# Kernel optimization log

Hardware: AMD Instinct MI355X
Metric: run time of the kernel (lower is better)

Reference implementation:

```python
import jax, jax.numpy as jnp
import numpy as np

ALPHA = 0.2  # LeakyReLU negative slope
NEG_INF = -9e15


def setup_inputs() -> dict:
    key = jax.random.key(0)
    k1, k2, k3, k4 = jax.random.split(key, 4)
    B, T, N, Fin, Fout = 16, 12, 512, 64, 64
    h = jax.random.normal(k1, (B, T, N, Fin), dtype=jnp.float32)
    adj = jax.random.randint(k2, (N, N), 0, 2).astype(jnp.float32)
    W = jax.random.normal(k3, (Fin, Fout), dtype=jnp.float32) * 0.1
    a = jax.random.normal(k4, (2 * Fout, 1), dtype=jnp.float32) * 0.1
    return {"h": h, "adj": adj, "W": W, "a": a}


def reference(h, adj, W, a):
    # h: [B,T,N,Fin], adj: [N,N], W: [Fin,Fout], a: [2*Fout,1]
    Fout = W.shape[1]
    Wh = jnp.einsum('btnf,fo->btno', h, W)          # [B,T,N,Fout]
    a1 = a[:Fout, 0]                                 # [Fout]
    a2 = a[Fout:, 0]                                 # [Fout]
    Wh1 = Wh @ a1                                    # [B,T,N]
    Wh2 = Wh @ a2                                    # [B,T,N]
    e = Wh1[..., :, None] + Wh2[..., None, :]        # [B,T,N,N]
    e = jnp.where(e > 0, e, ALPHA * e)               # LeakyReLU
    att = jnp.where(adj > 0, e, NEG_INF)             # adjacency mask (broadcast)
    att = jax.nn.softmax(att, axis=-1)
    # dropout is identity in eval mode (training=False)
    h_prime = jnp.einsum('btij,btjo->btio', att, Wh)  # [B,T,N,Fout]
    return jax.nn.elu(h_prime)                        # concat=True -> ELU
```

## Files before the change

### kernel.cpp

```cpp
#include <hip/hip_runtime.h>


typedef __attribute__((ext_vector_type(8))) short short8;
typedef __attribute__((ext_vector_type(4))) float f32x4;

union U16x8 { uint4 v; short8 s; };

static __device__ __forceinline__ f32x4 mfma16(short8 a, short8 b, f32x4 c) {
    return __builtin_amdgcn_mfma_f32_16x16x32_bf16(a, b, c, 0, 0, 0);
}

static __device__ __forceinline__ void pk_hilo(float x, float y,
                                               unsigned& hw, unsigned& lw) {
    asm("v_cvt_pk_bf16_f32 %0, %1, %2" : "=v"(hw) : "v"(x), "v"(y));
    float rx = x - __uint_as_float(hw << 16);
    float ry = y - __uint_as_float(hw & 0xffff0000u);
    asm("v_cvt_pk_bf16_f32 %0, %1, %2" : "=v"(lw) : "v"(rx), "v"(ry));
}

__global__ __launch_bounds__(512)
void adj_bits_kernel(const float* __restrict__ adj, unsigned long long* __restrict__ bits)
{
    const int tid  = threadIdx.x;
    const int lane = tid & 63;
    const int w    = tid >> 6;
    const int g    = blockIdx.x * 8 + w;
    const int row  = g >> 3;
    const int k    = g & 7;
    float v = adj[row * 512 + k * 64 + lane];
    unsigned long long m = __ballot(v > 0.f);
    if (lane == 0) bits[row * 8 + k] = m;
}

__global__ __launch_bounds__(1024, 4)
void gat_fused(const float* __restrict__ h, const float* __restrict__ W,
               const float* __restrict__ a,
               const unsigned long long* __restrict__ bits,
               float* __restrict__ out)
{
    __shared__ unsigned short WhH[64 * 512];
    __shared__ unsigned short WhL[64 * 512];
    __shared__ float wh1s[512];
    __shared__ float wh2s[512];
    __shared__ __align__(16) float e2p[512];
    __shared__ __align__(16) float e2n[512];

    const int tid  = threadIdx.x;
    const int lane = tid & 63;
    const int wv   = tid >> 6;
    const int col  = lane & 15;
    const int g    = lane >> 4;
    const int bt   = blockIdx.x;

    U16x8 WBh[2][4], WBl[2][4];
    #pragma unroll
    for (int kt = 0; kt < 2; ++kt) {
        #pragma unroll
        for (int ot = 0; ot < 4; ++ot) {
            const float* wp = &W[(kt * 32 + 8 * g) * 64 + ot * 16 + col];
            pk_hilo(wp[0],   wp[64],  WBh[kt][ot].v.x, WBl[kt][ot].v.x);
            pk_hilo(wp[128], wp[192], WBh[kt][ot].v.y, WBl[kt][ot].v.y);
            pk_hilo(wp[256], wp[320], WBh[kt][ot].v.z, WBl[kt][ot].v.z);
            pk_hilo(wp[384], wp[448], WBh[kt][ot].v.w, WBl[kt][ot].v.w);
        }
    }
    float a1c[4], a2c[4];
    #pragma unroll
    for (int ot = 0; ot < 4; ++ot) {
        a1c[ot] = a[ot * 16 + col];
        a2c[ot] = a[64 + ot * 16 + col];
    }

    #pragma unroll 1
    for (int mt = 0; mt < 2; ++mt) {
        const int n0w = wv * 32 + mt * 16;

        const float* hrow = &h[((size_t)bt * 512 + n0w + col) * 64];
        const float4 ha0 = *(const float4*)&hrow[8 * g];
        const float4 ha1 = *(const float4*)&hrow[8 * g + 4];
        const float4 hb0 = *(const float4*)&hrow[32 + 8 * g];
        const float4 hb1 = *(const float4*)&hrow[32 + 8 * g + 4];

        U16x8 A0h, A0l, A1h, A1l;
        pk_hilo(ha0.x, ha0.y, A0h.v.x, A0l.v.x);
        pk_hilo(ha0.z, ha0.w, A0h.v.y, A0l.v.y);
        pk_hilo(ha1.x, ha1.y, A0h.v.z, A0l.v.z);
        pk_hilo(ha1.z, ha1.w, A0h.v.w, A0l.v.w);
        pk_hilo(hb0.x, hb0.y, A1h.v.x, A1l.v.x);
        pk_hilo(hb0.z, hb0.w, A1h.v.y, A1l.v.y);
        pk_hilo(hb1.x, hb1.y, A1h.v.z, A1l.v.z);
        pk_hilo(hb1.z, hb1.w, A1h.v.w, A1l.v.w);

        f32x4 acc[4];
        #pragma unroll
        for (int ot = 0; ot < 4; ++ot) acc[ot] = (f32x4){0.f, 0.f, 0.f, 0.f};

        #pragma unroll
        for (int kt = 0; kt < 2; ++kt) {
            const short8 Ah = (kt == 0) ? A0h.s : A1h.s;
            const short8 Al = (kt == 0) ? A0l.s : A1l.s;
            #pragma unroll
            for (int ot = 0; ot < 4; ++ot) {
                acc[ot] = mfma16(Ah, WBh[kt][ot].s, acc[ot]);
                acc[ot] = mfma16(Al, WBh[kt][ot].s, acc[ot]);
                acc[ot] = mfma16(Ah, WBl[kt][ot].s, acc[ot]);
            }
        }

        #pragma unroll
        for (int r = 0; r < 4; ++r) {
            float t1 = acc[0][r] * a1c[0] + acc[1][r] * a1c[1]
                     + acc[2][r] * a1c[2] + acc[3][r] * a1c[3];
            float t2 = acc[0][r] * a2c[0] + acc[1][r] * a2c[1]
                     + acc[2][r] * a2c[2] + acc[3][r] * a2c[3];
            #pragma unroll
            for (int s = 1; s <= 8; s <<= 1) {
                t1 += __shfl_xor(t1, s);
                t2 += __shfl_xor(t2, s);
            }
            if (col == 0) {
                const int n = n0w + g * 4 + r;
                wh1s[n] = t1;
                wh2s[n] = t2;
            }
        }

        #pragma unroll
        for (int ot = 0; ot < 4; ++ot) {
            const int o = ot * 16 + col;
            unsigned h01, l01, h23, l23;
            pk_hilo(acc[ot][0], acc[ot][1], h01, l01);
            pk_hilo(acc[ot][2], acc[ot][3], h23, l23);
            const int gg = (n0w >> 3) + (g >> 1);
            const int pg = gg ^ (o & 7);
            const int el = o * 512 + pg * 8 + (g & 1) * 4;
            *(uint2*)&WhH[el] = make_uint2(h01, h23);
            *(uint2*)&WhL[el] = make_uint2(l01, l23);
        }
    }

    __syncthreads();

    if (tid < 512) {
        const float w2 = wh2s[tid];
        e2p[tid] = __expf(w2);
        e2n[tid] = __expf(0.2f * w2);
    }
    __syncthreads();

    const int rowb = wv * 32;
    float E1p[2], E1n[2], Tt[2];
    #pragma unroll
    for (int mt = 0; mt < 2; ++mt) {
        const float v = wh1s[rowb + mt * 16 + col];
        E1p[mt] = __expf(v);
        E1n[mt] = __expf(0.2f * v);
        Tt[mt]  = __expf(-v);
    }

    short8 ones;
    #pragma unroll
    for (int r = 0; r < 8; ++r) ones[r] = (short)0x3F80;

    f32x4 acc[2][4];
    f32x4 sacc[2];
    #pragma unroll
    for (int mt = 0; mt < 2; ++mt) {
        sacc[mt] = (f32x4){0.f, 0.f, 0.f, 0.f};
        #pragma unroll
        for (int ot = 0; ot < 4; ++ot) acc[mt][ot] = (f32x4){0.f, 0.f, 0.f, 0.f};
    }

    const unsigned* b32 = (const unsigned*)bits;
    const int row0 = rowb + col;
    const int row1 = row0 + 16;

    #pragma unroll 1
    for (int ko = 0; ko < 4; ++ko) {
        const uint4 wA4 = *(const uint4*)&b32[(size_t)row0 * 16 + ko * 4];
        const uint4 wB4 = *(const uint4*)&b32[(size_t)row1 * 16 + ko * 4];
        const unsigned wa[4] = {wA4.x, wA4.y, wA4.z, wA4.w};
        const unsigned wb[4] = {wB4.x, wB4.y, wB4.z, wB4.w};

        #pragma unroll
        for (int ki = 0; ki < 4; ++ki) {
            const int kk = ko * 4 + ki;
            const int k0 = kk * 32;

            const float4 epa = *(const float4*)&e2p[k0 + 8 * g];
            const float4 epb = *(const float4*)&e2p[k0 + 8 * g + 4];
            const float4 ena = *(const float4*)&e2n[k0 + 8 * g];
            const float4 enb = *(const float4*)&e2n[k0 + 8 * g + 4];
            const float ep8[8] = {epa.x, epa.y, epa.z, epa.w, epb.x, epb.y, epb.z, epb.w};
            const float en8[8] = {ena.x, ena.y, ena.z, ena.w, enb.x, enb.y, enb.z, enb.w};
            const unsigned mb0 = (wa[ki] >> (8 * g)) & 0xffu;
            const unsigned mb1 = (wb[ki] >> (8 * g)) & 0xffu;

            U16x8 Ah[2], Al[2];
            {
                float pv0[8], pv1[8];
                #pragma unroll
                for (int r = 0; r < 8; ++r) {
                    const bool c0 = ep8[r] > Tt[0];
                    float p0 = (c0 ? E1p[0] : E1n[0]) * (c0 ? ep8[r] : en8[r]);
                    pv0[r] = ((mb0 >> r) & 1u) ? p0 : 0.f;
                    const bool c1 = ep8[r] > Tt[1];
                    float p1 = (c1 ? E1p[1] : E1n[1]) * (c1 ? ep8[r] : en8[r]);
                    pv1[r] = ((mb1 >> r) & 1u) ? p1 : 0.f;
                }
                pk_hilo(pv0[0], pv0[1], Ah[0].v.x, Al[0].v.x);
                pk_hilo(pv0[2], pv0[3], Ah[0].v.y, Al[0].v.y);
                pk_hilo(pv0[4], pv0[5], Ah[0].v.z, Al[0].v.z);
                pk_hilo(pv0[6], pv0[7], Ah[0].v.w, Al[0].v.w);
                pk_hilo(pv1[0], pv1[1], Ah[1].v.x, Al[1].v.x);
                pk_hilo(pv1[2], pv1[3], Ah[1].v.y, Al[1].v.y);
                pk_hilo(pv1[4], pv1[5], Ah[1].v.z, Al[1].v.z);
                pk_hilo(pv1[6], pv1[7], Ah[1].v.w, Al[1].v.w);
            }

            sacc[0] = mfma16(Ah[0].s, ones, sacc[0]);
            sacc[0] = mfma16(Al[0].s, ones, sacc[0]);
            sacc[1] = mfma16(Ah[1].s, ones, sacc[1]);
            sacc[1] = mfma16(Al[1].s, ones, sacc[1]);

            #pragma unroll
            for (int ot = 0; ot < 4; ++ot) {
                const int o  = ot * 16 + col;
                const int el = o * 512 + (((kk * 4 + g) ^ (o & 7)) << 3);
                U16x8 Bh, Bl;
                Bh.v = *(const uint4*)&WhH[el];
                Bl.v = *(const uint4*)&WhL[el];
                acc[0][ot] = mfma16(Ah[0].s, Bh.s, acc[0][ot]);
                acc[0][ot] = mfma16(Al[0].s, Bh.s, acc[0][ot]);
                acc[0][ot] = mfma16(Ah[0].s, Bl.s, acc[0][ot]);
                acc[1][ot] = mfma16(Ah[1].s, Bh.s, acc[1][ot]);
                acc[1][ot] = mfma16(Al[1].s, Bh.s, acc[1][ot]);
                acc[1][ot] = mfma16(Ah[1].s, Bl.s, acc[1][ot]);
            }
        }
    }

    const size_t ob = (size_t)bt * 32768;
    #pragma unroll
    for (int mt = 0; mt < 2; ++mt) {
        float inv[4];
        #pragma unroll
        for (int r = 0; r < 4; ++r) inv[r] = 1.f / sacc[mt][r];
        #pragma unroll
        for (int ot = 0; ot < 4; ++ot) {
            #pragma unroll
            for (int r = 0; r < 4; ++r) {
                float v = acc[mt][ot][r] * inv[r];
                v = (v > 0.f) ? v : __expf(v) - 1.f;
                const int rowi = rowb + mt * 16 + g * 4 + r;
                out[ob + (size_t)rowi * 64 + ot * 16 + col] = v;
            }
        }
    }
}

extern "C" void kernel_launch(void* const* d_in, const int* in_sizes, int n_in,
                              void* d_out, int out_size, void* d_ws, size_t ws_size,
                              hipStream_t stream)
{
    const float* h   = (const float*)d_in[0];
    const float* adj = (const float*)d_in[1];
    const float* W   = (const float*)d_in[2];
    const float* a   = (const float*)d_in[3];
    float* out = (float*)d_out;

    unsigned long long* bits = (unsigned long long*)d_ws;

    adj_bits_kernel<<<512, 512, 0, stream>>>(adj, bits);
    gat_fused<<<192, 1024, 0, stream>>>(h, W, a, bits, out);
}
```

Before: 112.1 us.

## Switch split-precision MFMA from bf16 to fp16 and store Wh as single fp16

Replaces the bf16 hi/lo split MFMAs with fp16 MFMAs, using fp16 round-toward-zero packing for the split. Wh in LDS is now stored as a single fp16 value instead of a hi/lo pair. This halves LDS use and reads and drops one of the three MFMAs per product in the attention-times-Wh loop. The LeakyReLU branch select becomes a fmax of the two exponential products, and the occupancy hint in launch bounds is removed. The risks are fp16 range overflow or underflow in the exp products and lower precision in Wh.

```diff
diff --git a/kernel.cpp b/kernel.cpp
--- a/kernel.cpp
+++ b/kernel.cpp
@@ -1,21 +1,29 @@
 #include <hip/hip_runtime.h>
 
 
-typedef __attribute__((ext_vector_type(8))) short short8;
-typedef __attribute__((ext_vector_type(4))) float f32x4;
-
-union U16x8 { uint4 v; short8 s; };
-
-static __device__ __forceinline__ f32x4 mfma16(short8 a, short8 b, f32x4 c) {
-    return __builtin_amdgcn_mfma_f32_16x16x32_bf16(a, b, c, 0, 0, 0);
-}
-
-static __device__ __forceinline__ void pk_hilo(float x, float y,
-                                               unsigned& hw, unsigned& lw) {
-    asm("v_cvt_pk_bf16_f32 %0, %1, %2" : "=v"(hw) : "v"(x), "v"(y));
-    float rx = x - __uint_as_float(hw << 16);
-    float ry = y - __uint_as_float(hw & 0xffff0000u);
-    asm("v_cvt_pk_bf16_f32 %0, %1, %2" : "=v"(lw) : "v"(rx), "v"(ry));
+typedef __attribute__((ext_vector_type(8))) _Float16 f16x8;
+typedef __attribute__((ext_vector_type(2))) __fp16  h16x2;
+typedef __attribute__((ext_vector_type(4))) float   f32x4;
+
+union U16x8 { uint4 v; f16x8 h; };
+union U16x2 { unsigned u; h16x2 h; };
+
+static __device__ __forceinline__ f32x4 mfma16(f16x8 a, f16x8 b, f32x4 c) {
+    return __builtin_amdgcn_mfma_f32_16x16x32_f16(a, b, c, 0, 0, 0);
+}
+
+static __device__ __forceinline__ void pk16_hilo(float x, float y,
+                                                 unsigned& hw, unsigned& lw) {
+    U16x2 a; a.h = __builtin_amdgcn_cvt_pkrtz(x, y);
+    float rx = x - (float)a.h.x;
+    float ry = y - (float)a.h.y;
+    U16x2 b; b.h = __builtin_amdgcn_cvt_pkrtz(rx, ry);
+    hw = a.u;
+    lw = b.u;
+}
+static __device__ __forceinline__ unsigned pk16(float x, float y) {
+    U16x2 a; a.h = __builtin_amdgcn_cvt_pkrtz(x, y);
+    return a.u;
 }
 
 __global__ __launch_bounds__(512)
@@ -32,14 +40,13 @@
     if (lane == 0) bits[row * 8 + k] = m;
 }
 
-__global__ __launch_bounds__(1024, 4)
+__global__ __launch_bounds__(1024)
 void gat_fused(const float* __restrict__ h, const float* __restrict__ W,
                const float* __restrict__ a,
                const unsigned long long* __restrict__ bits,
                float* __restrict__ out)
 {
-    __shared__ unsigned short WhH[64 * 512];
-    __shared__ unsigned short WhL[64 * 512];
+    __shared__ unsigned short WhP[64 * 512];
     __shared__ float wh1s[512];
     __shared__ float wh2s[512];
     __shared__ __align__(16) float e2p[512];
@@ -58,10 +65,10 @@
         #pragma unroll
         for (int ot = 0; ot < 4; ++ot) {
             const float* wp = &W[(kt * 32 + 8 * g) * 64 + ot * 16 + col];
-            pk_hilo(wp[0],   wp[64],  WBh[kt][ot].v.x, WBl[kt][ot].v.x);
-            pk_hilo(wp[128], wp[192], WBh[kt][ot].v.y, WBl[kt][ot].v.y);
-            pk_hilo(wp[256], wp[320], WBh[kt][ot].v.z, WBl[kt][ot].v.z);
-            pk_hilo(wp[384], wp[448], WBh[kt][ot].v.w, WBl[kt][ot].v.w);
+            pk16_hilo(wp[0],   wp[64],  WBh[kt][ot].v.x, WBl[kt][ot].v.x);
+            pk16_hilo(wp[128], wp[192], WBh[kt][ot].v.y, WBl[kt][ot].v.y);
+            pk16_hilo(wp[256], wp[320], WBh[kt][ot].v.z, WBl[kt][ot].v.z);
+            pk16_hilo(wp[384], wp[448], WBh[kt][ot].v.w, WBl[kt][ot].v.w);
         }
     }
     float a1c[4], a2c[4];
@@ -82,14 +89,14 @@
         const float4 hb1 = *(const float4*)&hrow[32 + 8 * g + 4];
 
         U16x8 A0h, A0l, A1h, A1l;
-        pk_hilo(ha0.x, ha0.y, A0h.v.x, A0l.v.x);
-        pk_hilo(ha0.z, ha0.w, A0h.v.y, A0l.v.y);
-        pk_hilo(ha1.x, ha1.y, A0h.v.z, A0l.v.z);
-        pk_hilo(ha1.z, ha1.w, A0h.v.w, A0l.v.w);
-        pk_hilo(hb0.x, hb0.y, A1h.v.x, A1l.v.x);
-        pk_hilo(hb0.z, hb0.w, A1h.v.y, A1l.v.y);
-        pk_hilo(hb1.x, hb1.y, A1h.v.z, A1l.v.z);
-        pk_hilo(hb1.z, hb1.w, A1h.v.w, A1l.v.w);
+        pk16_hilo(ha0.x, ha0.y, A0h.v.x, A0l.v.x);
+        pk16_hilo(ha0.z, ha0.w, A0h.v.y, A0l.v.y);
+        pk16_hilo(ha1.x, ha1.y, A0h.v.z, A0l.v.z);
+        pk16_hilo(ha1.z, ha1.w, A0h.v.w, A0l.v.w);
+        pk16_hilo(hb0.x, hb0.y, A1h.v.x, A1l.v.x);
+        pk16_hilo(hb0.z, hb0.w, A1h.v.y, A1l.v.y);
+        pk16_hilo(hb1.x, hb1.y, A1h.v.z, A1l.v.z);
+        pk16_hilo(hb1.z, hb1.w, A1h.v.w, A1l.v.w);
 
         f32x4 acc[4];
         #pragma unroll
@@ -97,13 +104,13 @@
 
         #pragma unroll
         for (int kt = 0; kt < 2; ++kt) {
-            const short8 Ah = (kt == 0) ? A0h.s : A1h.s;
-            const short8 Al = (kt == 0) ? A0l.s : A1l.s;
+            const f16x8 Ah = (kt == 0) ? A0h.h : A1h.h;
+            const f16x8 Al = (kt == 0) ? A0l.h : A1l.h;
             #pragma unroll
             for (int ot = 0; ot < 4; ++ot) {
-                acc[ot] = mfma16(Ah, WBh[kt][ot].s, acc[ot]);
-                acc[ot] = mfma16(Al, WBh[kt][ot].s, acc[ot]);
-                acc[ot] = mfma16(Ah, WBl[kt][ot].s, acc[ot]);
+                acc[ot] = mfma16(Ah, WBh[kt][ot].h, acc[ot]);
+                acc[ot] = mfma16(Al, WBh[kt][ot].h, acc[ot]);
+                acc[ot] = mfma16(Ah, WBl[kt][ot].h, acc[ot]);
             }
         }
 
@@ -128,14 +135,12 @@
         #pragma unroll
         for (int ot = 0; ot < 4; ++ot) {
             const int o = ot * 16 + col;
-            unsigned h01, l01, h23, l23;
-            pk_hilo(acc[ot][0], acc[ot][1], h01, l01);
-            pk_hilo(acc[ot][2], acc[ot][3], h23, l23);
+            const unsigned w01 = pk16(acc[ot][0], acc[ot][1]);
+            const unsigned w23 = pk16(acc[ot][2], acc[ot][3]);
             const int gg = (n0w >> 3) + (g >> 1);
             const int pg = gg ^ (o & 7);
             const int el = o * 512 + pg * 8 + (g & 1) * 4;
-            *(uint2*)&WhH[el] = make_uint2(h01, h23);
-            *(uint2*)&WhL[el] = make_uint2(l01, l23);
+            *(uint2*)&WhP[el] = make_uint2(w01, w23);
         }
     }
 
@@ -149,18 +154,17 @@
     __syncthreads();
 
     const int rowb = wv * 32;
-    float E1p[2], E1n[2], Tt[2];
+    float E1p[2], E1n[2];
     #pragma unroll
     for (int mt = 0; mt < 2; ++mt) {
         const float v = wh1s[rowb + mt * 16 + col];
         E1p[mt] = __expf(v);
         E1n[mt] = __expf(0.2f * v);
-        Tt[mt]  = __expf(-v);
-    }
-
-    short8 ones;
-    #pragma unroll
-    for (int r = 0; r < 8; ++r) ones[r] = (short)0x3F80;
+    }
+
+    f16x8 ones;
+    #pragma unroll
+    for (int r = 0; r < 8; ++r) ones[r] = (_Float16)1.0f;
 
     f32x4 acc[2][4];
     f32x4 sacc[2];
@@ -201,41 +205,35 @@
                 float pv0[8], pv1[8];
                 #pragma unroll
                 for (int r = 0; r < 8; ++r) {
-                    const bool c0 = ep8[r] > Tt[0];
-                    float p0 = (c0 ? E1p[0] : E1n[0]) * (c0 ? ep8[r] : en8[r]);
+                    float p0 = fmaxf(E1p[0] * ep8[r], E1n[0] * en8[r]);
                     pv0[r] = ((mb0 >> r) & 1u) ? p0 : 0.f;
-                    const bool c1 = ep8[r] > Tt[1];
-                    float p1 = (c1 ? E1p[1] : E1n[1]) * (c1 ? ep8[r] : en8[r]);
+                    float p1 = fmaxf(E1p[1] * ep8[r], E1n[1] * en8[r]);
                     pv1[r] = ((mb1 >> r) & 1u) ? p1 : 0.f;
                 }
-                pk_hilo(pv0[0], pv0[1], Ah[0].v.x, Al[0].v.x);
-                pk_hilo(pv0[2], pv0[3], Ah[0].v.y, Al[0].v.y);
-                pk_hilo(pv0[4], pv0[5], Ah[0].v.z, Al[0].v.z);
-                pk_hilo(pv0[6], pv0[7], Ah[0].v.w, Al[0].v.w);
-                pk_hilo(pv1[0], pv1[1], Ah[1].v.x, Al[1].v.x);
-                pk_hilo(pv1[2], pv1[3], Ah[1].v.y, Al[1].v.y);
-                pk_hilo(pv1[4], pv1[5], Ah[1].v.z, Al[1].v.z);
-                pk_hilo(pv1[6], pv1[7], Ah[1].v.w, Al[1].v.w);
-            }
-
-            sacc[0] = mfma16(Ah[0].s, ones, sacc[0]);
-            sacc[0] = mfma16(Al[0].s, ones, sacc[0]);
-            sacc[1] = mfma16(Ah[1].s, ones, sacc[1]);
-            sacc[1] = mfma16(Al[1].s, ones, sacc[1]);
+                pk16_hilo(pv0[0], pv0[1], Ah[0].v.x, Al[0].v.x);
+                pk16_hilo(pv0[2], pv0[3], Ah[0].v.y, Al[0].v.y);
+                pk16_hilo(pv0[4], pv0[5], Ah[0].v.z, Al[0].v.z);
+                pk16_hilo(pv0[6], pv0[7], Ah[0].v.w, Al[0].v.w);
+                pk16_hilo(pv1[0], pv1[1], Ah[1].v.x, Al[1].v.x);
+                pk16_hilo(pv1[2], pv1[3], Ah[1].v.y, Al[1].v.y);
+                pk16_hilo(pv1[4], pv1[5], Ah[1].v.z, Al[1].v.z);
+                pk16_hilo(pv1[6], pv1[7], Ah[1].v.w, Al[1].v.w);
+            }
+
+            sacc[0] = mfma16(Ah[0].h, ones, sacc[0]);
+            sacc[0] = mfma16(Al[0].h, ones, sacc[0]);
+            sacc[1] = mfma16(Ah[1].h, ones, sacc[1]);
+            sacc[1] = mfma16(Al[1].h, ones, sacc[1]);
 
             #pragma unroll
             for (int ot = 0; ot < 4; ++ot) {
                 const int o  = ot * 16 + col;
                 const int el = o * 512 + (((kk * 4 + g) ^ (o & 7)) << 3);
-                U16x8 Bh, Bl;
-                Bh.v = *(const uint4*)&WhH[el];
-                Bl.v = *(const uint4*)&WhL[el];
-                acc[0][ot] = mfma16(Ah[0].s, Bh.s, acc[0][ot]);
-                acc[0][ot] = mfma16(Al[0].s, Bh.s, acc[0][ot]);
-                acc[0][ot] = mfma16(Ah[0].s, Bl.s, acc[0][ot]);
-                acc[1][ot] = mfma16(Ah[1].s, Bh.s, acc[1][ot]);
-                acc[1][ot] = mfma16(Al[1].s, Bh.s, acc[1][ot]);
-                acc[1][ot] = mfma16(Ah[1].s, Bl.s, acc[1][ot]);
+                U16x8 B; B.v = *(const uint4*)&WhP[el];
+                acc[0][ot] = mfma16(Ah[0].h, B.h, acc[0][ot]);
+                acc[0][ot] = mfma16(Al[0].h, B.h, acc[0][ot]);
+                acc[1][ot] = mfma16(Ah[1].h, B.h, acc[1][ot]);
+                acc[1][ot] = mfma16(Al[1].h, B.h, acc[1][ot]);
             }
         }
     }
```

After: 109.6 us. -2.3%, faster.
